# Optimization experiments

Hardware: AMD Instinct MI355X
Metric: run time of the kernel (lower is better)

Reference implementation:

```python
import jax, jax.numpy as jnp
import numpy as np

B, G, C = 32, 512, 768
BG = B * G
H = 12              # MHA heads
MID, H1, N1 = 12, 6, 128   # Attention1 mid dim, heads, fixed block size
AD = 16             # adapter bottleneck
FF = 4 * C
NCLUST = 2048       # 3d grid cells
GRID = 196
D1 = B * GRID       # 1d scatter dim_size
NVIEW = 6
SCALE_FACTOR = 0.5
COEF_PRO = 0.3
EPS = 1e-5


def layernorm(x, g, b):
    m = x.mean(-1, keepdims=True)
    v = x.var(-1, keepdims=True)
    return (x - m) / jnp.sqrt(v + EPS) * g + b


def quick_gelu(x):
    return x * jax.nn.sigmoid(1.702 * x)


def bn_gelu(x, g, b):
    # BatchNorm1d in training mode (batch statistics, biased var) + exact GELU
    m = x.mean(0)
    v = x.var(0)
    y = (x - m) / jnp.sqrt(v + EPS) * g + b
    return jax.nn.gelu(y, approximate=False)


def seg_max_mean(feat, idx, nseg):
    # segment_csr(sorted feat, ptr) == segment reduce over cluster ids; empty segments -> 0
    cnt = jax.ops.segment_sum(jnp.ones((feat.shape[0], 1), feat.dtype), idx, nseg)
    smax = jnp.where(cnt > 0, jax.ops.segment_max(feat, idx, nseg), 0.0)
    smean = jax.ops.segment_sum(feat, idx, nseg) / jnp.maximum(cnt, 1.0)
    return smax, smean


def setup_inputs() -> dict:
    key = jax.random.key(0)
    ks = iter(jax.random.split(key, 40))
    r = lambda shape, s=0.02: jax.random.normal(next(ks), shape, jnp.float32) * s
    return {
        "x": jax.random.normal(next(ks), (B, G + 1, C), jnp.float32),
        "ln1_g": jnp.ones((C,)), "ln1_b": jnp.zeros((C,)),
        "ln2_g": jnp.ones((C,)), "ln2_b": jnp.zeros((C,)),
        "Wqkv": r((3 * C, C)), "bqkv": jnp.zeros((3 * C,)),
        "Wo": r((C, C)), "bo": jnp.zeros((C,)),
        "Wfc": r((FF, C)), "bfc": jnp.zeros((FF,)),
        "Wproj": r((C, FF)), "bproj": jnp.zeros((C,)),
        "Wa1": r((AD, C)), "ba1": jnp.zeros((AD,)),
        "Wa2": r((C, AD)), "ba2": jnp.zeros((C,)),
        "bn3d_g": jnp.ones((C,)), "bn3d_b": jnp.zeros((C,)),
        "bn1d_g": jnp.ones((NVIEW, C)), "bn1d_b": jnp.zeros((NVIEW, C)),
        "n3_g": jnp.ones((NVIEW, C)), "n3_b": jnp.zeros((NVIEW, C)),
        "a1_qkv_w": r((NVIEW, 3 * MID, C)), "a1_qkv_b": jnp.zeros((NVIEW, 3 * MID)),
        "a1_proj_w": r((NVIEW, C, MID)), "a1_proj_b": jnp.zeros((NVIEW, C)),
        "cluster": jax.random.randint(next(ks), (BG,), 0, NCLUST),
        "flat_grid_index": jax.random.randint(next(ks), (NVIEW, BG), 0, D1),
        "mask": jax.random.randint(next(ks), (NVIEW, BG // N1, N1, N1), 0, 2).astype(bool),
    }


def reference(x, ln1_g, ln1_b, ln2_g, ln2_b, Wqkv, bqkv, Wo, bo, Wfc, bfc,
              Wproj, bproj, Wa1, ba1, Wa2, ba2, bn3d_g, bn3d_b, bn1d_g, bn1d_b,
              n3_g, n3_b, a1_qkv_w, a1_qkv_b, a1_proj_w, a1_proj_b,
              cluster, flat_grid_index, mask):
    hd = C // H
    # --- multi-head self-attention over tokens + residual ---
    y = layernorm(x, ln1_g, ln1_b)
    qkv = y @ Wqkv.T + bqkv                          # [B, S, 3C]
    q, k, v = jnp.split(qkv, 3, axis=-1)
    heads = lambda t: t.reshape(B, G + 1, H, hd).transpose(0, 2, 1, 3)
    q, k, v = heads(q), heads(k), heads(v)
    attn = jax.nn.softmax(jnp.einsum('bhqd,bhkd->bhqk', q, k) / jnp.sqrt(jnp.float32(hd)), axis=-1)
    o = jnp.einsum('bhqk,bhkd->bhqd', attn, v).transpose(0, 2, 1, 3).reshape(B, G + 1, C)
    x = x + o @ Wo.T + bo
    # --- MLP (QuickGELU) + scaled adapter ---
    y = layernorm(x, ln2_g, ln2_b)
    x_ffn = quick_gelu(y @ Wfc.T + bfc) @ Wproj.T + bproj
    adapt = quick_gelu(x_ffn @ Wa1.T + ba1) @ Wa2.T + ba2
    x = x + x_ffn + SCALE_FACTOR * adapt
    cls_x = x[:, :1]
    xt = x[:, 1:]                                    # [B, G, C]
    feat = xt.reshape(BG, C)
    # --- 3d cluster pooling: segment max+mean -> BN+GELU -> gather back ---
    fmax, fmean = seg_max_mean(feat, cluster, NCLUST)
    x_3d = bn_gelu(fmax + fmean, bn3d_g, bn3d_b)[cluster].reshape(B, G, C)
    # --- per-view local masked attention + 1d grid scatter pooling (vmapped) ---
    def view_branch(n3g, n3b, qkvw, qkvb, projw, projb, bng, bnb, idx, msk):
        z = layernorm(feat, n3g, n3b)
        qkv1 = (z @ qkvw.T + qkvb).reshape(BG // N1, N1, 3, H1, MID // H1).transpose(2, 0, 3, 1, 4)
        q1, k1, v1 = qkv1[0], qkv1[1], qkv1[2]       # [Bn, H1, N1, hd1]
        a = jnp.einsum('bhqd,bhkd->bhqk', q1, k1) * (MID ** -0.5)
        a = a + jnp.where(msk, -100000.0, 0.0)[:, None]  # mask broadcast over heads
        a = jax.nn.softmax(a, axis=-1)
        o1 = jnp.einsum('bhqk,bhkd->bhqd', a, v1).transpose(0, 2, 1, 3).reshape(BG, MID)
        flat = o1 @ projw.T + projb + feat
        smax, smean = seg_max_mean(flat, idx, D1)
        return bn_gelu(smax + smean, bng, bnb)[idx].reshape(B, G, C)
    pos = jax.vmap(view_branch)(n3_g, n3_b, a1_qkv_w, a1_qkv_b, a1_proj_w, a1_proj_b,
                                bn1d_g, bn1d_b, flat_grid_index, mask)   # [6, B, G, C]
    # --- cosine-similarity-weighted fusion of the 6 views against x_3d ---
    def cossim(a, b):
        na = jnp.maximum(jnp.linalg.norm(a, axis=-1), 1e-8)
        nb = jnp.maximum(jnp.linalg.norm(b, axis=-1), 1e-8)
        return (a * b).sum(-1) / (na * nb)
    sims = (jax.vmap(lambda p: cossim(p, x_3d))(pos) + 1.0) / 2.0        # [6, B, G]
    sims = sims / sims.sum(0, keepdims=True)
    x_sup = (pos * sims[..., None]).sum(0)                               # [B, G, C]
    xt = xt + COEF_PRO * x_sup
    return jnp.concatenate([cls_x, xt], axis=1)
```

## Files before the change

kernel.cpp:

```cpp
#include <hip/hip_runtime.h>
#include <hip/hip_bf16.h>
#include <math.h>

typedef unsigned int u32;
typedef __hip_bfloat16 bf16;
typedef __attribute__((ext_vector_type(8))) short bh8;
typedef __attribute__((ext_vector_type(4))) float fx4;
typedef __attribute__((ext_vector_type(2))) unsigned int u32x2;
typedef __attribute__((ext_vector_type(4))) unsigned int u32x4;

#define CDIM   768
#define BATCH  32
#define SEQ    513
#define NT     (BATCH*SEQ)
#define NR     16384
#define NHEAD  12
#define HD     64
#define FFDIM  3072
#define NCLUST 2048
#define D1SEG  6272
#define NVIEW  6
#define MIDD   12
#define H1N    6
#define N1V    128
#define NB1    128
#define CHROWS 8208

#define A_FS      ((size_t)0)
#define B_FS      ((size_t)6303744)
#define X1_FS     ((size_t)25214976)
#define AH_FS     ((size_t)31518720)
#define D_FS      ((size_t)31781376)
#define DTOT_FS   9640064
#define X3D_FS    ((size_t)(D_FS + DTOT_FS))
#define BNV_FS    (X3D_FS + 1572864)
#define STATM_FS  (BNV_FS + 14450688)
#define STATR_FS  (STATM_FS + 768)
#define DI_CNT    (D_FS)
#define DI_BASE   (D_FS + 6272)
#define DI_CUR    (D_FS + 12544)
#define DI_ORD    (D_FS + 18816)
#define DW_FS     (D_FS + 40960)
#define DWV_FS    (D_FS + 3600000)

__device__ inline float b2f(bf16 v){ return __bfloat162float(v); }
__device__ inline float ldv(const float* p, size_t i){ return p[i]; }
__device__ inline float ldv(const bf16*  p, size_t i){ return __bfloat162float(p[i]); }
__device__ inline void  stv(float* p, size_t i, float v){ p[i] = v; }
__device__ inline void  stv(bf16*  p, size_t i, float v){ p[i] = __float2bfloat16(v); }
__device__ inline short f2bs(float f){ bf16 h = __float2bfloat16(f); return *(short*)&h; }
__device__ inline void gload_lds16(const bf16* g, short* l){
    __builtin_amdgcn_global_load_lds((const __attribute__((address_space(1))) void*)g,
                                     (__attribute__((address_space(3))) void*)l, 16, 0, 0);
}
__device__ inline u32x2 ds_tr16(unsigned a){
    u32x2 d;
    asm volatile("ds_read_b64_tr_b16 %0, %1" : "=v"(d) : "v"(a));
    return d;
}


__global__ __launch_bounds__(256) void k_zero(float* p, int n){
    for (int i = blockIdx.x*256 + threadIdx.x; i < n; i += gridDim.x*256) p[i] = 0.0f;
}

__global__ __launch_bounds__(256) void k_f2b(const float* __restrict__ in, bf16* __restrict__ out, int n){
    for (int i = blockIdx.x*256 + threadIdx.x; i < n; i += gridDim.x*256)
        out[i] = __float2bfloat16(in[i]);
}

template<typename TI>
__global__ __launch_bounds__(256) void k_ln(const TI* __restrict__ in, bf16* __restrict__ out,
                                            const float* __restrict__ g, const float* __restrict__ b){
    int i = blockIdx.x;
    int tid = threadIdx.x;
    const TI* r = in + (size_t)i*CDIM;
    float v0 = ldv(r,(size_t)tid), v1 = ldv(r,(size_t)tid+256), v2 = ldv(r,(size_t)tid+512);
    float s  = v0+v1+v2;
    float s2 = v0*v0+v1*v1+v2*v2;
    __shared__ float t1[4], t2[4];
    #pragma unroll
    for (int o=32;o;o>>=1){ s += __shfl_down(s,o,64); s2 += __shfl_down(s2,o,64); }
    int lane = tid & 63, wid = tid >> 6;
    if (!lane){ t1[wid]=s; t2[wid]=s2; }
    __syncthreads();
    float S  = t1[0]+t1[1]+t1[2]+t1[3];
    float S2 = t2[0]+t2[1]+t2[2]+t2[3];
    float m  = S * (1.0f/CDIM);
    float var = S2 * (1.0f/CDIM) - m*m;
    float rstd = rsqrtf(var + 1e-5f);
    bf16* o_ = out + (size_t)i*CDIM;
    stv(o_,(size_t)tid,     (v0-m)*rstd*g[tid]     + b[tid]);
    stv(o_,(size_t)tid+256, (v1-m)*rstd*g[tid+256] + b[tid+256]);
    stv(o_,(size_t)tid+512, (v2-m)*rstd*g[tid+512] + b[tid+512]);
}

__global__ __launch_bounds__(256) void k_lnn(const float* __restrict__ in, bf16* __restrict__ out){
    int i = blockIdx.x;
    size_t ri = (size_t)(i + (i>>9) + 1);
    int tid = threadIdx.x;
    const float* r = in + ri*CDIM;
    float v0 = r[tid], v1 = r[tid+256], v2 = r[tid+512];
    float s  = v0+v1+v2;
    float s2 = v0*v0+v1*v1+v2*v2;
    __shared__ float t1[4], t2[4];
    #pragma unroll
    for (int o=32;o;o>>=1){ s += __shfl_down(s,o,64); s2 += __shfl_down(s2,o,64); }
    int lane = tid & 63, wid = tid >> 6;
    if (!lane){ t1[wid]=s; t2[wid]=s2; }
    __syncthreads();
    float S  = t1[0]+t1[1]+t1[2]+t1[3];
    float S2 = t2[0]+t2[1]+t2[2]+t2[3];
    float m  = S * (1.0f/CDIM);
    float var = S2 * (1.0f/CDIM) - m*m;
    float rstd = rsqrtf(var + 1e-5f);
    bf16* o_ = out + (size_t)i*CDIM;
    stv(o_,(size_t)tid,     (v0-m)*rstd);
    stv(o_,(size_t)tid+256, (v1-m)*rstd);
    stv(o_,(size_t)tid+512, (v2-m)*rstd);
}

__global__ __launch_bounds__(256) void k_foldw(const float* __restrict__ aqw, const float* __restrict__ aqb,
                                               const float* __restrict__ n3g, const float* __restrict__ n3b,
                                               bf16* __restrict__ Wv, float* __restrict__ bv){
    int row = blockIdx.x;
    int v = row/36;
    const float* w = aqw + (size_t)row*768;
    const float* g = n3g + v*768;
    const float* b = n3b + v*768;
    int tid = threadIdx.x;
    float s = 0.0f;
    #pragma unroll
    for (int j=tid; j<768; j+=256){
        float wv = w[j];
        Wv[(size_t)row*768 + j] = __float2bfloat16(wv*g[j]);
        s += wv*b[j];
    }
    __shared__ float t1[4];
    #pragma unroll
    for (int o=32;o;o>>=1) s += __shfl_down(s,o,64);
    int lane = tid & 63, wid = tid >> 6;
    if (!lane) t1[wid]=s;
    __syncthreads();
    if (tid==0) bv[row] = aqb[row] + t1[0]+t1[1]+t1[2]+t1[3];
}

template<typename TO, int ACT, int RES>
__global__ __launch_bounds__(256) void k_gemm_mfma(const bf16* __restrict__ A, const bf16* __restrict__ W,
                                                   const float* __restrict__ bias, const float* __restrict__ res,
                                                   TO* __restrict__ out, int M, int N, int K){
    __shared__ short As[3][128*32];
    __shared__ short Ws[3][128*32];
    int nbx = (N + 127) >> 7;
    int nwg = gridDim.x;
    int orig = blockIdx.x;
    int xcd = orig & 7, sl = orig >> 3;
    int q8 = nwg >> 3, r8 = nwg & 7;
    int wg = (xcd < r8 ? xcd*(q8+1) : r8*(q8+1) + (xcd - r8)*q8) + sl;
    int by = wg / nbx;
    int bm = by*128, bn = (wg - by*nbx)*128;
    int tid = threadIdx.x, wid = tid>>6, lane = tid&63, quad = lane>>4, l16 = lane&15;
    int wr = (wid>>1)*64, wc = (wid&1)*64;
    fx4 acc[4][4];
    #pragma unroll
    for (int i=0;i<4;i++)
        #pragma unroll
        for (int j=0;j<4;j++) acc[i][j] = (fx4){0.f,0.f,0.f,0.f};
    int lrow = lane>>2;
    int gchunk = (lane&3) ^ ((lane>>3)&3);
    int r0a0 = wid*32 + lrow,  r0a1 = wid*32 + 16 + lrow;
    int ra0 = bm + r0a0; if (ra0 > M-1) ra0 = M-1;
    int ra1 = bm + r0a1; if (ra1 > M-1) ra1 = M-1;
    int rw0 = bn + r0a0; if (rw0 > N-1) rw0 = N-1;
    int rw1 = bn + r0a1; if (rw1 > N-1) rw1 = N-1;
    const bf16* pa0 = A + (size_t)ra0*K + gchunk*8;
    const bf16* pa1 = A + (size_t)ra1*K + gchunk*8;
    const bf16* pw0 = W + (size_t)rw0*K + gchunk*8;
    const bf16* pw1 = W + (size_t)rw1*K + gchunk*8;
    int sL0 = (wid*32)*32;
    int sL1 = (wid*32 + 16)*32;
    int slotx = (l16>>1)&3;
    int nt = K >> 5;
    #define STAGE4(bsel, t) do { int _k0 = (t) << 5;               \
        gload_lds16(pa0 + _k0, &As[(bsel)][sL0]);                  \
        gload_lds16(pa1 + _k0, &As[(bsel)][sL1]);                  \
        gload_lds16(pw0 + _k0, &Ws[(bsel)][sL0]);                  \
        gload_lds16(pw1 + _k0, &Ws[(bsel)][sL1]); } while(0)
    STAGE4(0, 0);
    STAGE4(1, 1);
    int cur = 0;
    for (int t = 0; t < nt; ++t){
        if (t + 1 < nt) asm volatile("s_waitcnt vmcnt(4)" ::: "memory");
        else            asm volatile("s_waitcnt vmcnt(0)" ::: "memory");
        __builtin_amdgcn_s_barrier();
        __builtin_amdgcn_sched_barrier(0);
        const short* Ab = &As[cur][0];
        const short* Wb = &Ws[cur][0];
        bh8 af[4], bf_[4];
        int sa = (quad ^ slotx)*8;
        #pragma unroll
        for (int i=0;i<4;i++) af[i]  = *(const bh8*)&Ab[(wr + i*16 + l16)*32 + sa];
        #pragma unroll
        for (int j=0;j<4;j++) bf_[j] = *(const bh8*)&Wb[(wc + j*16 + l16)*32 + sa];
        if (t + 2 < nt){
            int nb = cur + 2; if (nb >= 3) nb -= 3;
            STAGE4(nb, t + 2);
        }
        #pragma unroll
        for (int i=0;i<4;i++)
            #pragma unroll
            for (int j=0;j<4;j++)
                acc[i][j] = __builtin_amdgcn_mfma_f32_16x16x32_bf16(af[i], bf_[j], acc[i][j], 0,0,0);
        cur += 1; if (cur == 3) cur = 0;
    }
    #undef STAGE4
    #pragma unroll
    for (int i=0;i<4;i++){
        #pragma unroll
        for (int r=0;r<4;r++){
            int row = bm + wr + i*16 + quad*4 + r;
            if (row >= M) continue;
            #pragma unroll
            for (int j=0;j<4;j++){
                int col = bn + wc + j*16 + l16;
                if (col >= N) continue;
                float v = acc[i][j][r] + bias[col];
                if (ACT == 1) v = v / (1.0f + __expf(-1.702f*v));
                if (RES) v += res[(size_t)row*N + col];
                stv(out, (size_t)row*N + col, v);
            }
        }
    }
}

#define KSTR 72
__global__ __launch_bounds__(256) void k_attn_mfma(const bf16* __restrict__ qkv, bf16* __restrict__ obuf){
    __shared__ short Ks[2][64*KSTR];
    __shared__ short Vs[2][64*KSTR];
    __shared__ short Ps[4*16*KSTR];
    int id = blockIdx.x;
    int qt = (id>>3) % 9;
    int bh = (id&7) + ((id/72)<<3);
    int h = bh % NHEAD, b = bh / NHEAD;
    int tid = threadIdx.x, wid = tid>>6, lane = tid&63, quad = lane>>4, l16 = lane&15;
    size_t base = (size_t)b*SEQ*2304;
    int q_own = qt*64 + wid*16 + l16;
    int q_cl  = q_own > 512 ? 512 : q_own;
    const bf16* qrow = qkv + base + (size_t)q_cl*2304 + h*HD;
    bh8 qa0 = *(const bh8*)(qrow + quad*8);
    bh8 qa1 = *(const bh8*)(qrow + 32 + quad*8);
    {
        union { bh8 v; short s[8]; } u0, u1;
        u0.v = qa0; u1.v = qa1;
        #pragma unroll
        for (int j=0;j<8;j++){
            bf16 a = *(bf16*)&u0.s[j]; u0.s[j] = f2bs(0.125f*b2f(a));
            bf16 c = *(bf16*)&u1.s[j]; u1.s[j] = f2bs(0.125f*b2f(c));
        }
        qa0 = u0.v; qa1 = u1.v;
    }
    fx4 o[4];
    #pragma unroll
    for (int d=0; d<4; d++) o[d] = (fx4){0.f,0.f,0.f,0.f};
    float mrow[4] = {-1e30f,-1e30f,-1e30f,-1e30f};
    float lrow[4] = {0.f,0.f,0.f,0.f};
    int srow = tid>>2, d0 = (tid&3)*16;
    int s_st = (srow>>2)*4 + (tid&3);
    int vsb  = (s_st ^ ((srow>>3)<<1))*KSTR + (srow&3)*16;
    int h8 = l16>>3, l7 = l16&7;
    short* psw[4];
    #pragma unroll
    for (int nt=0;nt<4;nt++)
        psw[nt] = &Ps[(wid*16 + quad*4)*KSTR + (((nt<<1)|h8) ^ (quad<<1))*8 + l7];
    int swr = (l16>>2)<<1;
    const short* prd0 = &Ps[(wid*16+l16)*KSTR + ((quad ^ swr))*8];
    const short* prd1 = &Ps[(wid*16+l16)*KSTR + (((4|quad) ^ swr))*8];
    unsigned vls = (unsigned)(size_t)(__attribute__((address_space(3))) short*)&Vs[0][0] + 2u*l16;
    #define TRA(vb,hf,c,dt) ((vb) + 144u*(unsigned)(((32*(hf) + 8*quad + 4*(c) + (dt)) ^ (8*(hf) + 2*quad))))
    bh8 kv0, kv1, vv0, vv1;
    {
        const bf16* krow = qkv + base + 768 + (size_t)srow*2304 + h*HD + d0;
        kv0 = *(const bh8*)(krow);
        kv1 = *(const bh8*)(krow + 8);
        vv0 = *(const bh8*)(krow + 768);
        vv1 = *(const bh8*)(krow + 776);
    }
    int p = 0;
    for (int kt=0; kt<9; kt++){
        short* KsP = &Ks[p][0];
        short* VsP = &Vs[p][0];
        *(bh8*)&KsP[srow*KSTR + d0]     = kv0;
        *(bh8*)&KsP[srow*KSTR + d0 + 8] = kv1;
        *(bh8*)&VsP[vsb]     = vv0;
        *(bh8*)&VsP[vsb + 8] = vv1;
        __syncthreads();
        if (kt < 8){
            int kg = (kt+1)*64 + srow; if (kg > 512) kg = 512;
            const bf16* krow = qkv + base + 768 + (size_t)kg*2304 + h*HD + d0;
            kv0 = *(const bh8*)(krow);
            kv1 = *(const bh8*)(krow + 8);
            vv0 = *(const bh8*)(krow + 768);
            vv1 = *(const bh8*)(krow + 776);
        }
        unsigned vb = vls + 9216u*(unsigned)p;
        fx4 s[4];
        __builtin_amdgcn_s_setprio(1);
        #pragma unroll
        for (int nt=0; nt<4; nt++){
            bh8 kb0 = *(const bh8*)&KsP[(nt*16+l16)*KSTR + quad*8];
            bh8 kb1 = *(const bh8*)&KsP[(nt*16+l16)*KSTR + 32 + quad*8];
            fx4 a = (fx4){0.f,0.f,0.f,0.f};
            a = __builtin_amdgcn_mfma_f32_16x16x32_bf16(qa0, kb0, a, 0,0,0);
            a = __builtin_amdgcn_mfma_f32_16x16x32_bf16(qa1, kb1, a, 0,0,0);
            s[nt] = a;
        }
        __builtin_amdgcn_s_setprio(0);
        u32x2 tv[16];
        #pragma unroll
        for (int dt=0; dt<4; dt++){
            tv[dt*4+0] = ds_tr16(TRA(vb,0,0,dt));
            tv[dt*4+1] = ds_tr16(TRA(vb,0,1,dt));
            tv[dt*4+2] = ds_tr16(TRA(vb,1,0,dt));
            tv[dt*4+3] = ds_tr16(TRA(vb,1,1,dt));
        }
        float tmax[4] = {-1e30f,-1e30f,-1e30f,-1e30f};
        if (kt < 8){
            #pragma unroll
            for (int nt=0; nt<4; nt++)
                #pragma unroll
                for (int r=0;r<4;r++) tmax[r] = fmaxf(tmax[r], s[nt][r]);
        } else {
            #pragma unroll
            for (int nt=0; nt<4; nt++){
                bool ok = (nt==0) && (l16==0);
                #pragma unroll
                for (int r=0;r<4;r++){
                    float v = ok ? s[nt][r] : -1e30f;
                    s[nt][r] = v;
                    tmax[r] = fmaxf(tmax[r], v);
                }
            }
        }
        #pragma unroll
        for (int msk=1; msk<16; msk<<=1)
            #pragma unroll
            for (int r=0;r<4;r++) tmax[r] = fmaxf(tmax[r], __shfl_xor(tmax[r], msk, 64));
        bool grow = (tmax[0]>mrow[0])|(tmax[1]>mrow[1])|(tmax[2]>mrow[2])|(tmax[3]>mrow[3]);
        if (__any(grow)){
            #pragma unroll
            for (int r=0;r<4;r++){
                float mn = fmaxf(mrow[r], tmax[r]);
                float al = __expf(mrow[r] - mn);
                mrow[r] = mn;
                lrow[r] *= al;
                #pragma unroll
                for (int d=0; d<4; d++) o[d][r] *= al;
            }
        }
        float ps[4] = {0.f,0.f,0.f,0.f};
        #pragma unroll
        for (int nt=0; nt<4; nt++)
            #pragma unroll
            for (int r=0;r<4;r++){
                float pp = __expf(s[nt][r] - mrow[r]);
                s[nt][r] = pp;
                ps[r] += pp;
            }
        #pragma unroll
        for (int msk=1; msk<16; msk<<=1)
            #pragma unroll
            for (int r=0;r<4;r++) ps[r] += __shfl_xor(ps[r], msk, 64);
        #pragma unroll
        for (int r=0;r<4;r++) lrow[r] += ps[r];
        #pragma unroll
        for (int nt=0; nt<4; nt++)
            #pragma unroll
            for (int r=0;r<4;r++) psw[nt][r*KSTR] = f2bs(s[nt][r]);
        bh8 pa0 = *(const bh8*)prd0;
        bh8 pa1 = *(const bh8*)prd1;
        asm volatile("s_waitcnt lgkmcnt(0)" ::: "memory");
        __builtin_amdgcn_sched_barrier(0);
        __builtin_amdgcn_s_setprio(1);
        #pragma unroll
        for (int dt=0; dt<4; dt++){
            union { u32x4 u; bh8 h; } v0, v1;
            v0.u = (u32x4){tv[dt*4+0][0], tv[dt*4+0][1], tv[dt*4+1][0], tv[dt*4+1][1]};
            v1.u = (u32x4){tv[dt*4+2][0], tv[dt*4+2][1], tv[dt*4+3][0], tv[dt*4+3][1]};
            o[dt] = __builtin_amdgcn_mfma_f32_16x16x32_bf16(pa0, v0.h, o[dt], 0,0,0);
            o[dt] = __builtin_amdgcn_mfma_f32_16x16x32_bf16(pa1, v1.h, o[dt], 0,0,0);
        }
        __builtin_amdgcn_s_setprio(0);
        p ^= 1;
    }
    #undef TRA
    float inv[4];
    #pragma unroll
    for (int r=0;r<4;r++) inv[r] = 1.0f/lrow[r];
    #pragma unroll
    for (int r=0;r<4;r++){
        int q = qt*64 + wid*16 + quad*4 + r;
        if (q < SEQ){
            size_t ob = ((size_t)(b*SEQ+q))*CDIM + h*HD;
            #pragma unroll
            for (int dt=0; dt<4; dt++)
                obuf[ob + dt*16 + l16] = __float2bfloat16(o[dt][r]*inv[r]);
        }
    }
}

__global__ __launch_bounds__(256) void k_comb(const bf16* __restrict__ x1, const bf16* __restrict__ xffn,
                                              const float* __restrict__ ah, const float* __restrict__ Wa2,
                                              const float* __restrict__ ba2, float* __restrict__ x2){
    int i = blockIdx.x; int tid = threadIdx.x;
    __shared__ float ar[16];
    if (tid < 16) ar[tid] = ah[(size_t)i*16 + tid];
    __syncthreads();
    for (int c=tid; c<CDIM; c+=256){
        const float* w = Wa2 + (size_t)c*16;
        float a = ba2[c];
        #pragma unroll
        for (int mm=0; mm<16; mm++) a += ar[mm]*w[mm];
        size_t o = (size_t)i*CDIM + c;
        x2[o] = b2f(x1[o]) + b2f(xffn[o]) + 0.5f*a;
    }
}

__global__ __launch_bounds__(256) void k_icount(const int* __restrict__ idx, int* __restrict__ cnt, int n){
    int i = blockIdx.x*256 + threadIdx.x;
    if (i < n) atomicAdd(&cnt[idx[i]], 1);
}

__global__ __launch_bounds__(256) void k_iscan(const int* __restrict__ cnt, int* __restrict__ base,
                                               int* __restrict__ cur, int nseg){
    __shared__ int part[256], off[256];
    int t = threadIdx.x;
    int chunk = (nseg + 255) >> 8;
    int j0 = t*chunk, j1 = j0 + chunk; if (j1 > nseg) j1 = nseg;
    int s = 0;
    for (int j=j0; j<j1; j++) s += cnt[j];
    part[t] = s; __syncthreads();
    if (t == 0){ int acc=0; for (int i=0;i<256;i++){ off[i]=acc; acc+=part[i]; } }
    __syncthreads();
    int acc = off[t];
    for (int j=j0; j<j1; j++){ base[j]=acc; cur[j]=acc; acc+=cnt[j]; }
}

__global__ __launch_bounds__(256) void k_iscatter(const int* __restrict__ idx, int* __restrict__ cur,
                                                  int* __restrict__ order, int n){
    int i = blockIdx.x*256 + threadIdx.x;
    if (i < n){
        int pos = atomicAdd(&cur[idx[i]], 1);
        order[pos] = i;
    }
}

__global__ __launch_bounds__(256) void k_icount6(const int* __restrict__ fgi, int* __restrict__ cnt){
    int g = blockIdx.x*256 + threadIdx.x;
    int v = g >> 14;
    atomicAdd(&cnt[v*D1SEG + fgi[g]], 1);
}

__global__ __launch_bounds__(256) void k_iscan6(const int* __restrict__ cnt, int* __restrict__ base,
                                                int* __restrict__ cur){
    __shared__ int part[256], off[256];
    int v = blockIdx.x;
    const int* c = cnt + v*D1SEG;
    int* bs = base + v*D1SEG;
    int* cu = cur + v*D1SEG;
    int t = threadIdx.x;
    int chunk = (D1SEG + 255) >> 8;
    int j0 = t*chunk, j1 = j0 + chunk; if (j1 > D1SEG) j1 = D1SEG;
    int s = 0;
    for (int j=j0; j<j1; j++) s += c[j];
    part[t] = s; __syncthreads();
    if (t == 0){ int acc=0; for (int i=0;i<256;i++){ off[i]=acc; acc+=part[i]; } }
    __syncthreads();
    int acc = off[t];
    for (int j=j0; j<j1; j++){ bs[j]=acc; cu[j]=acc; acc+=c[j]; }
}

__global__ __launch_bounds__(256) void k_iscatter6(const int* __restrict__ fgi, int* __restrict__ cur,
                                                   int* __restrict__ order){
    int g = blockIdx.x*256 + threadIdx.x;
    int v = g >> 14;
    int pos = atomicAdd(&cur[v*D1SEG + fgi[g]], 1);
    order[(size_t)v*NR + pos] = g & (NR-1);
}

__global__ __launch_bounds__(256) void k_gather_seg(const float* __restrict__ outx, const int* __restrict__ basep,
                                                    const int* __restrict__ cntp, const int* __restrict__ order,
                                                    float* __restrict__ dst){
    int sg = blockIdx.x; int tid = threadIdx.x;
    int n = cntp[sg], b0 = basep[sg];
    float mx[3] = {-1e30f,-1e30f,-1e30f};
    float sm[3] = {0.f,0.f,0.f};
    for (int r=0; r<n; r++){
        int i = order[b0+r];
        size_t rb = (size_t)(i + (i>>9) + 1)*CDIM;
        #pragma unroll
        for (int j=0;j<3;j++){
            float v = outx[rb + tid + j*256];
            mx[j] = fmaxf(mx[j], v); sm[j] += v;
        }
    }
    float den = (float)(n > 1 ? n : 1);
    size_t db = (size_t)sg*CDIM;
    #pragma unroll
    for (int j=0;j<3;j++)
        dst[db + tid + j*256] = (n > 0 ? mx[j] : 0.f) + sm[j]/den;
}

__global__ __launch_bounds__(256) void k_gather_flat(const float* __restrict__ outx, const float* __restrict__ o1v,
                                                     const float* __restrict__ Wp, const float* __restrict__ bp,
                                                     const int* __restrict__ basep, const int* __restrict__ cntp,
                                                     const int* __restrict__ order, float* __restrict__ dst){
    int sg = blockIdx.x; int tid = threadIdx.x;
    int n = cntp[sg], b0 = basep[sg];
    float w[3][MIDD], bb[3];
    #pragma unroll
    for (int j=0;j<3;j++){
        int c = tid + j*256;
        bb[j] = bp[c];
        #pragma unroll
        for (int mm=0;mm<MIDD;mm++) w[j][mm] = Wp[(size_t)c*MIDD + mm];
    }
    float mx[3] = {-1e30f,-1e30f,-1e30f};
    float sm[3] = {0.f,0.f,0.f};
    for (int r=0; r<n; r++){
        int i = order[b0+r];
        const float* orow = o1v + (size_t)i*MIDD;
        float ov[MIDD];
        #pragma unroll
        for (int mm=0;mm<MIDD;mm++) ov[mm] = orow[mm];
        size_t rb = (size_t)(i + (i>>9) + 1)*CDIM;
        #pragma unroll
        for (int j=0;j<3;j++){
            float a = bb[j];
            #pragma unroll
            for (int mm=0;mm<MIDD;mm++) a += ov[mm]*w[j][mm];
            a += outx[rb + tid + j*256];
            mx[j] = fmaxf(mx[j], a); sm[j] += a;
        }
    }
    float den = (float)(n > 1 ? n : 1);
    size_t db = (size_t)sg*CDIM;
    #pragma unroll
    for (int j=0;j<3;j++)
        dst[db + tid + j*256] = (n > 0 ? mx[j] : 0.f) + sm[j]/den;
}

__global__ __launch_bounds__(256) void k_colstats_part(const float* __restrict__ in, int rows,
                                                       float* __restrict__ sumv, float* __restrict__ sumsq){
    int c = blockIdx.x*256 + threadIdx.x;
    if (c >= CDIM) return;
    int chunk = (rows + 31) >> 5;
    int r0 = blockIdx.y*chunk;
    int r1 = r0 + chunk; if (r1 > rows) r1 = rows;
    float s = 0.0f, s2 = 0.0f;
    for (int r=r0; r<r1; r++){
        float v = in[(size_t)r*CDIM + c];
        s += v; s2 += v*v;
    }
    atomicAdd(&sumv[c], s);
    atomicAdd(&sumsq[c], s2);
}

template<typename TO>
__global__ __launch_bounds__(256) void k_bngelu2(const float* __restrict__ in, TO* __restrict__ outp,
                                                 const float* __restrict__ sv, const float* __restrict__ sq,
                                                 const float* __restrict__ g, const float* __restrict__ b,
                                                 int n, float invn){
    int i = blockIdx.x*256 + threadIdx.x;
    if (i >= n) return;
    int c = i - (i/CDIM)*CDIM;
    float m = sv[c]*invn;
    float var = sq[c]*invn - m*m;
    float r = rsqrtf(fmaxf(var, 0.0f) + 1e-5f);
    float y = (in[i]-m)*r*g[c] + b[c];
    stv(outp, (size_t)i, 0.5f*y*(1.0f + erff(y*0.70710678118654752f)));
}

#define MSTR 33
__global__ __launch_bounds__(256) void k_attnv(const float* __restrict__ qkv1a,
                                               const unsigned char* __restrict__ mask,
                                               float* __restrict__ o1all){
    __shared__ float Qs[N1V][13], Ksv[N1V][13], Vsv[N1V][13];
    __shared__ int   Ms[N1V*MSTR];
    int blk = blockIdx.x, v = blockIdx.y;
    int tid = threadIdx.x;
    if (tid < N1V){
        const float4* rp = (const float4*)(qkv1a + (size_t)(blk*N1V + tid)*216 + v*36);
        #pragma unroll
        for (int j=0;j<3;j++){
            float4 q4 = rp[j], k4 = rp[3+j], v4 = rp[6+j];
            Qs[tid][j*4+0]=q4.x; Qs[tid][j*4+1]=q4.y; Qs[tid][j*4+2]=q4.z; Qs[tid][j*4+3]=q4.w;
            Ksv[tid][j*4+0]=k4.x; Ksv[tid][j*4+1]=k4.y; Ksv[tid][j*4+2]=k4.z; Ksv[tid][j*4+3]=k4.w;
            Vsv[tid][j*4+0]=v4.x; Vsv[tid][j*4+1]=v4.y; Vsv[tid][j*4+2]=v4.z; Vsv[tid][j*4+3]=v4.w;
        }
    }
    {
        const int4* mp = (const int4*)(mask + ((size_t)v*NB1 + blk)*N1V*N1V);
        #pragma unroll
        for (int it=0; it<4; it++){
            int e = tid + it*256;
            int4 m4 = mp[e];
            int row = e >> 3, c4 = (e & 7)*4;
            Ms[row*MSTR + c4 + 0] = m4.x;
            Ms[row*MSTR + c4 + 1] = m4.y;
            Ms[row*MSTR + c4 + 2] = m4.z;
            Ms[row*MSTR + c4 + 3] = m4.w;
        }
    }
    __syncthreads();
    int n = tid & 127, hg = tid >> 7;
    const float scale = 0.28867513459481287f;
    #pragma unroll
    for (int hh=0; hh<3; hh++){
        int h = hg*3 + hh;
        float q0 = Qs[n][h*2], q1 = Qs[n][h*2+1];
        float m = -1e30f;
        #pragma unroll 4
        for (int k4=0; k4<32; k4++){
            int mw = Ms[n*MSTR + k4];
            #pragma unroll
            for (int j=0;j<4;j++){
                int k = k4*4 + j;
                float s = (q0*Ksv[k][h*2] + q1*Ksv[k][h*2+1])*scale + (((mw>>(j*8))&0xFF) ? -100000.0f : 0.0f);
                m = fmaxf(m, s);
            }
        }
        float l = 0.f, o0 = 0.f, o1v = 0.f;
        #pragma unroll 4
        for (int k4=0; k4<32; k4++){
            int mw = Ms[n*MSTR + k4];
            #pragma unroll
            for (int j=0;j<4;j++){
                int k = k4*4 + j;
                float s = (q0*Ksv[k][h*2] + q1*Ksv[k][h*2+1])*scale + (((mw>>(j*8))&0xFF) ? -100000.0f : 0.0f);
                float p = __expf(s - m);
                l += p; o0 += p*Vsv[k][h*2]; o1v += p*Vsv[k][h*2+1];
            }
        }
        float inv = 1.0f/l;
        float* orow = o1all + ((size_t)v*NR + blk*N1V + n)*MIDD + h*2;
        orow[0] = o0*inv; orow[1] = o1v*inv;
    }
}

__global__ __launch_bounds__(256) void k_final(float* __restrict__ outx, const float* __restrict__ x3d,
                                               const bf16* __restrict__ bnv, const int* __restrict__ cluster,
                                               const int* __restrict__ fgi){
    int i = blockIdx.x; int tid = threadIdx.x;
    int cl = cluster[i];
    const float* xr = x3d + (size_t)cl*CDIM;
    const bf16* pr[NVIEW];
    #pragma unroll
    for (int v=0; v<NVIEW; v++)
        pr[v] = bnv + ((size_t)v*D1SEG + fgi[(size_t)v*NR + i])*CDIM;
    size_t rb = (size_t)(i + (i>>9) + 1)*CDIM;
    float pv[NVIEW][3], ft[3];
    float dotv[NVIEW] = {0,0,0,0,0,0};
    float np2[NVIEW]  = {0,0,0,0,0,0};
    float nx2 = 0.0f;
    #pragma unroll
    for (int j=0; j<3; j++){
        int c = tid + j*256;
        float xv = xr[c]; nx2 += xv*xv;
        ft[j] = outx[rb + c];
        #pragma unroll
        for (int v=0; v<NVIEW; v++){
            float p = b2f(pr[v][c]); pv[v][j] = p;
            dotv[v] += p*xv; np2[v] += p*p;
        }
    }
    __shared__ float part[4*13];
    __shared__ float ssim[NVIEW];
    float vals[13];
    vals[0] = nx2;
    #pragma unroll
    for (int v=0; v<NVIEW; v++){ vals[1+v] = dotv[v]; vals[7+v] = np2[v]; }
    int lane = tid & 63, wid = tid >> 6;
    #pragma unroll
    for (int k=0; k<13; k++){
        float w = vals[k];
        #pragma unroll
        for (int o=32;o;o>>=1) w += __shfl_down(w,o,64);
        if (!lane) part[wid*13 + k] = w;
    }
    __syncthreads();
    if (tid == 0){
        float tot[13];
        #pragma unroll
        for (int k=0; k<13; k++) tot[k] = part[k] + part[13+k] + part[26+k] + part[39+k];
        float nb = fmaxf(sqrtf(tot[0]), 1e-8f);
        float sv[NVIEW]; float ssumv = 0.0f;
        #pragma unroll
        for (int v=0; v<NVIEW; v++){
            float na = fmaxf(sqrtf(tot[7+v]), 1e-8f);
            float cs = tot[1+v] / (na*nb);
            sv[v] = (cs + 1.0f)*0.5f;
            ssumv += sv[v];
        }
        #pragma unroll
        for (int v=0; v<NVIEW; v++) ssim[v] = sv[v]/ssumv;
    }
    __syncthreads();
    #pragma unroll
    for (int j=0; j<3; j++){
        int c = tid + j*256;
        float xs = 0.0f;
        #pragma unroll
        for (int v=0; v<NVIEW; v++) xs += ssim[v]*pv[v][j];
        outx[rb + c] = ft[j] + 0.3f*xs;
    }
}

extern "C" void kernel_launch(void* const* d_in, const int* in_sizes, int n_in,
                              void* d_out, int out_size, void* d_ws, size_t ws_size,
                              hipStream_t stream){
    const float* x     = (const float*)d_in[0];
    const float* ln1g  = (const float*)d_in[1];
    const float* ln1b  = (const float*)d_in[2];
    const float* ln2g  = (const float*)d_in[3];
    const float* ln2b  = (const float*)d_in[4];
    const float* Wqkv  = (const float*)d_in[5];
    const float* bqkv  = (const float*)d_in[6];
    const float* Wo    = (const float*)d_in[7];
    const float* bo    = (const float*)d_in[8];
    const float* Wfc   = (const float*)d_in[9];
    const float* bfc   = (const float*)d_in[10];
    const float* Wproj = (const float*)d_in[11];
    const float* bproj = (const float*)d_in[12];
    const float* Wa1   = (const float*)d_in[13];
    const float* ba1   = (const float*)d_in[14];
    const float* Wa2   = (const float*)d_in[15];
    const float* ba2   = (const float*)d_in[16];
    const float* bn3dg = (const float*)d_in[17];
    const float* bn3db = (const float*)d_in[18];
    const float* bn1dg = (const float*)d_in[19];
    const float* bn1db = (const float*)d_in[20];
    const float* n3g   = (const float*)d_in[21];
    const float* n3b   = (const float*)d_in[22];
    const float* aqw   = (const float*)d_in[23];
    const float* aqb   = (const float*)d_in[24];
    const float* apw   = (const float*)d_in[25];
    const float* apb   = (const float*)d_in[26];
    const int*   cluster = (const int*)d_in[27];
    const int*   fgi     = (const int*)d_in[28];
    const unsigned char* mask = (const unsigned char*)d_in[29];
    float* out = (float*)d_out;
    float* ws  = (float*)d_ws;

    bf16*  yb    = (bf16*)(ws + A_FS);
    bf16*  qkvb  = (bf16*)(ws + B_FS);
    bf16*  hb    = (bf16*)(ws + B_FS);
    bf16*  xffb  = (bf16*)(ws + B_FS + 12607488);
    float* qkv1a = ws + B_FS;
    float* o1all = ws + B_FS + 3538944;
    float* svs   = ws + B_FS + 4718592;
    bf16*  x1b   = (bf16*)(ws + X1_FS);
    float* ah    = ws + AH_FS;
    int*   icnt  = (int*)(ws + DI_CNT);
    int*   ibase = (int*)(ws + DI_BASE);
    int*   icur  = (int*)(ws + DI_CUR);
    int*   iord  = (int*)(ws + DI_ORD);
    float* x3d   = ws + X3D_FS;
    bf16*  bnv   = (bf16*)(ws + BNV_FS);
    float* statm = ws + STATM_FS;
    float* statr = ws + STATR_FS;
    bf16* WqkvB  = (bf16*)(ws + DW_FS);
    bf16* WoB    = WqkvB + 2304*768;
    bf16* WfcB   = WoB   + 768*768;
    bf16* WprojB = WfcB  + 3072*768;
    bf16* WvB    = (bf16*)(ws + DWV_FS);
    float* bvP   = ws + DWV_FS + 82944;
    bf16* Wa1B   = (bf16*)(ws + DWV_FS + 83200);
    int*   icnt6  = (int*)(ws + AH_FS);
    int*   ibase6 = icnt6 + 6*D1SEG;
    int*   icur6  = ibase6 + 6*D1SEG;
    int*   iord6  = icur6 + 6*D1SEG;
    float* stat6  = (float*)(iord6 + 6*NR);

    k_f2b<<<1024, 256, 0, stream>>>(Wqkv,  WqkvB,  2304*768);
    k_f2b<<<1024, 256, 0, stream>>>(Wo,    WoB,    768*768);
    k_f2b<<<1024, 256, 0, stream>>>(Wfc,   WfcB,   3072*768);
    k_f2b<<<1024, 256, 0, stream>>>(Wproj, WprojB, 768*3072);
    k_f2b<<<48, 256, 0, stream>>>(Wa1, Wa1B, 16*768);
    k_foldw<<<216, 256, 0, stream>>>(aqw, aqb, n3g, n3b, WvB, bvP);
    k_ln<float><<<NT, 256, 0, stream>>>(x, yb, ln1g, ln1b);
    k_gemm_mfma<bf16,0,0><<<(2304/128)*((NT+127)/128), 256, 0, stream>>>(yb, WqkvB, bqkv, nullptr, qkvb, NT, 2304, 768);
    k_attn_mfma<<<3456, 256, 0, stream>>>(qkvb, yb);
    k_gemm_mfma<bf16,0,1><<<(768/128)*((NT+127)/128), 256, 0, stream>>>(yb, WoB, bo, x, x1b, NT, 768, 768);
    k_ln<bf16><<<NT, 256, 0, stream>>>(x1b, yb, ln2g, ln2b);
    for (int cch=0; cch<2; cch++){
        const bf16* a2 = yb + (size_t)cch*CHROWS*CDIM;
        bf16* xo = xffb + (size_t)cch*CHROWS*CDIM;
        k_gemm_mfma<bf16,1,0><<<(FFDIM/128)*((CHROWS+127)/128), 256, 0, stream>>>(a2, WfcB, bfc, nullptr, hb, CHROWS, FFDIM, 768);
        k_gemm_mfma<bf16,0,0><<<(768/128)*((CHROWS+127)/128), 256, 0, stream>>>(hb, WprojB, bproj, nullptr, xo, CHROWS, 768, FFDIM);
    }
    k_gemm_mfma<float,1,0><<<1*((NT+127)/128), 256, 0, stream>>>(xffb, Wa1B, ba1, nullptr, ah, NT, 16, 768);
    k_comb<<<NT, 256, 0, stream>>>(x1b, xffb, ah, Wa2, ba2, out);
    k_zero<<<32, 256, 0, stream>>>((float*)icnt, NCLUST);
    k_icount<<<NR/256, 256, 0, stream>>>(cluster, icnt, NR);
    k_iscan<<<1, 256, 0, stream>>>(icnt, ibase, icur, NCLUST);
    k_iscatter<<<NR/256, 256, 0, stream>>>(cluster, icur, iord, NR);
    k_gather_seg<<<NCLUST, 256, 0, stream>>>(out, ibase, icnt, iord, x3d);
    k_zero<<<6, 256, 0, stream>>>(statm, 1536);
    k_colstats_part<<<dim3(3, 32), 256, 0, stream>>>(x3d, NCLUST, statm, statr);
    k_bngelu2<float><<<(NCLUST*CDIM+255)/256, 256, 0, stream>>>(x3d, x3d, statm, statr, bn3dg, bn3db,
                                                                NCLUST*CDIM, 1.0f/NCLUST);
    k_lnn<<<NR, 256, 0, stream>>>(out, yb);
    k_gemm_mfma<float,0,0><<<2*(NR/128), 256, 0, stream>>>(yb, WvB, bvP, nullptr, qkv1a, NR, 216, 768);
    k_attnv<<<dim3(NB1, NVIEW), 256, 0, stream>>>(qkv1a, mask, o1all);
    k_zero<<<(6*D1SEG+255)/256, 256, 0, stream>>>((float*)icnt6, 6*D1SEG);
    k_icount6<<<6*NR/256, 256, 0, stream>>>(fgi, icnt6);
    k_iscan6<<<6, 256, 0, stream>>>(icnt6, ibase6, icur6);
    k_iscatter6<<<6*NR/256, 256, 0, stream>>>(fgi, icur6, iord6);
    k_zero<<<(9216+255)/256, 256, 0, stream>>>(stat6, 9216);
    for (int v=0; v<NVIEW; v++){
        k_gather_flat<<<D1SEG, 256, 0, stream>>>(out, o1all + (size_t)v*NR*MIDD,
                                                 apw + (size_t)v*CDIM*MIDD, apb + (size_t)v*CDIM,
                                                 ibase6 + v*D1SEG, icnt6 + v*D1SEG, iord6 + (size_t)v*NR, svs);
        k_colstats_part<<<dim3(3, 32), 256, 0, stream>>>(svs, D1SEG, stat6 + v*1536, stat6 + v*1536 + 768);
        k_bngelu2<bf16><<<(D1SEG*CDIM+255)/256, 256, 0, stream>>>(svs, bnv + (size_t)v*D1SEG*CDIM,
                                                                  stat6 + v*1536, stat6 + v*1536 + 768,
                                                                  bn1dg + v*CDIM, bn1db + v*CDIM,
                                                                  D1SEG*CDIM, 1.0f/D1SEG);
    }
    k_final<<<NR, 256, 0, stream>>>(out, x3d, bnv, cluster, fgi);
}
```

Measured before the change: 1.597 ms.

## Transpose attention scores to simplify softmax, merge conversion and zero launches

```diff
diff --git a/kernel.cpp b/kernel.cpp
--- a/kernel.cpp
+++ b/kernel.cpp
@@ -58,15 +58,28 @@
     asm volatile("ds_read_b64_tr_b16 %0, %1" : "=v"(d) : "v"(a));
     return d;
 }
+__device__ inline unsigned cvtpk_bf16(float lo, float hi){
+    unsigned r;
+    asm("v_cvt_pk_bf16_f32 %0, %1, %2" : "=v"(r) : "v"(lo), "v"(hi));
+    return r;
+}
 
 
 __global__ __launch_bounds__(256) void k_zero(float* p, int n){
     for (int i = blockIdx.x*256 + threadIdx.x; i < n; i += gridDim.x*256) p[i] = 0.0f;
 }
 
-__global__ __launch_bounds__(256) void k_f2b(const float* __restrict__ in, bf16* __restrict__ out, int n){
-    for (int i = blockIdx.x*256 + threadIdx.x; i < n; i += gridDim.x*256)
-        out[i] = __float2bfloat16(in[i]);
+__global__ __launch_bounds__(256) void k_f2b5(const float* __restrict__ a0, bf16* __restrict__ b0, int n0,
+                                              const float* __restrict__ a1, bf16* __restrict__ b1, int n1,
+                                              const float* __restrict__ a2, bf16* __restrict__ b2, int n2,
+                                              const float* __restrict__ a3, bf16* __restrict__ b3, int n3,
+                                              const float* __restrict__ a4, bf16* __restrict__ b4, int n4){
+    int i0 = blockIdx.x*256 + threadIdx.x, st = gridDim.x*256;
+    for (int i=i0; i<n0; i+=st) b0[i] = __float2bfloat16(a0[i]);
+    for (int i=i0; i<n1; i+=st) b1[i] = __float2bfloat16(a1[i]);
+    for (int i=i0; i<n2; i+=st) b2[i] = __float2bfloat16(a2[i]);
+    for (int i=i0; i<n3; i+=st) b3[i] = __float2bfloat16(a3[i]);
+    for (int i=i0; i<n4; i+=st) b4[i] = __float2bfloat16(a4[i]);
 }
 
 template<typename TI>
@@ -194,6 +207,10 @@
         else            asm volatile("s_waitcnt vmcnt(0)" ::: "memory");
         __builtin_amdgcn_s_barrier();
         __builtin_amdgcn_sched_barrier(0);
+        if (t + 2 < nt){
+            int nb = cur + 2; if (nb >= 3) nb -= 3;
+            STAGE4(nb, t + 2);
+        }
         const short* Ab = &As[cur][0];
         const short* Wb = &Ws[cur][0];
         bh8 af[4], bf_[4];
@@ -202,10 +219,6 @@
         for (int i=0;i<4;i++) af[i]  = *(const bh8*)&Ab[(wr + i*16 + l16)*32 + sa];
         #pragma unroll
         for (int j=0;j<4;j++) bf_[j] = *(const bh8*)&Wb[(wc + j*16 + l16)*32 + sa];
-        if (t + 2 < nt){
-            int nb = cur + 2; if (nb >= 3) nb -= 3;
-            STAGE4(nb, t + 2);
-        }
         #pragma unroll
         for (int i=0;i<4;i++)
             #pragma unroll
@@ -262,19 +275,13 @@
     fx4 o[4];
     #pragma unroll
     for (int d=0; d<4; d++) o[d] = (fx4){0.f,0.f,0.f,0.f};
-    float mrow[4] = {-1e30f,-1e30f,-1e30f,-1e30f};
-    float lrow[4] = {0.f,0.f,0.f,0.f};
+    float mrow = -1e30f, lrow = 0.f;
     int srow = tid>>2, d0 = (tid&3)*16;
     int s_st = (srow>>2)*4 + (tid&3);
     int vsb  = (s_st ^ ((srow>>3)<<1))*KSTR + (srow&3)*16;
-    int h8 = l16>>3, l7 = l16&7;
-    short* psw[4];
-    #pragma unroll
-    for (int nt=0;nt<4;nt++)
-        psw[nt] = &Ps[(wid*16 + quad*4)*KSTR + (((nt<<1)|h8) ^ (quad<<1))*8 + l7];
-    int swr = (l16>>2)<<1;
-    const short* prd0 = &Ps[(wid*16+l16)*KSTR + ((quad ^ swr))*8];
-    const short* prd1 = &Ps[(wid*16+l16)*KSTR + (((4|quad) ^ swr))*8];
+    short* pw = &Ps[(wid*16 + l16)*KSTR];
+    const short* prd0 = &Ps[(wid*16+l16)*KSTR + quad*8];
+    const short* prd1 = &Ps[(wid*16+l16)*KSTR + 32 + quad*8];
     unsigned vls = (unsigned)(size_t)(__attribute__((address_space(3))) short*)&Vs[0][0] + 2u*l16;
     #define TRA(vb,hf,c,dt) ((vb) + 144u*(unsigned)(((32*(hf) + 8*quad + 4*(c) + (dt)) ^ (8*(hf) + 2*quad))))
     bh8 kv0, kv1, vv0, vv1;
@@ -310,8 +317,8 @@
             bh8 kb0 = *(const bh8*)&KsP[(nt*16+l16)*KSTR + quad*8];
             bh8 kb1 = *(const bh8*)&KsP[(nt*16+l16)*KSTR + 32 + quad*8];
             fx4 a = (fx4){0.f,0.f,0.f,0.f};
-            a = __builtin_amdgcn_mfma_f32_16x16x32_bf16(qa0, kb0, a, 0,0,0);
-            a = __builtin_amdgcn_mfma_f32_16x16x32_bf16(qa1, kb1, a, 0,0,0);
+            a = __builtin_amdgcn_mfma_f32_16x16x32_bf16(kb0, qa0, a, 0,0,0);
+            a = __builtin_amdgcn_mfma_f32_16x16x32_bf16(kb1, qa1, a, 0,0,0);
             s[nt] = a;
         }
         __builtin_amdgcn_s_setprio(0);
@@ -323,59 +330,54 @@
             tv[dt*4+2] = ds_tr16(TRA(vb,1,0,dt));
             tv[dt*4+3] = ds_tr16(TRA(vb,1,1,dt));
         }
-        float tmax[4] = {-1e30f,-1e30f,-1e30f,-1e30f};
-        if (kt < 8){
+        if (kt == 8){
             #pragma unroll
             for (int nt=0; nt<4; nt++)
                 #pragma unroll
-                for (int r=0;r<4;r++) tmax[r] = fmaxf(tmax[r], s[nt][r]);
-        } else {
-            #pragma unroll
-            for (int nt=0; nt<4; nt++){
-                bool ok = (nt==0) && (l16==0);
+                for (int r=0;r<4;r++){
+                    bool ok = (nt==0) && (r==0) && (quad==0);
+                    s[nt][r] = ok ? s[nt][r] : -1e30f;
+                }
+        }
+        float ml = s[0][0];
+        #pragma unroll
+        for (int nt=0; nt<4; nt++)
+            #pragma unroll
+            for (int r=0;r<4;r++) if (nt|r) ml = fmaxf(ml, s[nt][r]);
+        ml = fmaxf(ml, __shfl_xor(ml, 16, 64));
+        ml = fmaxf(ml, __shfl_xor(ml, 32, 64));
+        if (__any(ml > mrow)){
+            float mn = fmaxf(mrow, ml);
+            float al = __expf(mrow - mn);
+            mrow = mn;
+            lrow *= al;
+            float alr[4];
+            #pragma unroll
+            for (int r=0;r<4;r++) alr[r] = __shfl(al, quad*4 + r, 16);
+            #pragma unroll
+            for (int d=0; d<4; d++)
                 #pragma unroll
-                for (int r=0;r<4;r++){
-                    float v = ok ? s[nt][r] : -1e30f;
-                    s[nt][r] = v;
-                    tmax[r] = fmaxf(tmax[r], v);
-                }
+                for (int r=0;r<4;r++) o[d][r] *= alr[r];
+        }
+        float ps = 0.f;
+        #pragma unroll
+        for (int nt=0; nt<4; nt++)
+            #pragma unroll
+            for (int r=0;r<4;r++){
+                float pp = __expf(s[nt][r] - mrow);
+                s[nt][r] = pp;
+                ps += pp;
             }
-        }
-        #pragma unroll
-        for (int msk=1; msk<16; msk<<=1)
-            #pragma unroll
-            for (int r=0;r<4;r++) tmax[r] = fmaxf(tmax[r], __shfl_xor(tmax[r], msk, 64));
-        bool grow = (tmax[0]>mrow[0])|(tmax[1]>mrow[1])|(tmax[2]>mrow[2])|(tmax[3]>mrow[3]);
-        if (__any(grow)){
-            #pragma unroll
-            for (int r=0;r<4;r++){
-                float mn = fmaxf(mrow[r], tmax[r]);
-                float al = __expf(mrow[r] - mn);
-                mrow[r] = mn;
-                lrow[r] *= al;
-                #pragma unroll
-                for (int d=0; d<4; d++) o[d][r] *= al;
-            }
-        }
-        float ps[4] = {0.f,0.f,0.f,0.f};
-        #pragma unroll
-        for (int nt=0; nt<4; nt++)
-            #pragma unroll
-            for (int r=0;r<4;r++){
-                float pp = __expf(s[nt][r] - mrow[r]);
-                s[nt][r] = pp;
-                ps[r] += pp;
-            }
-        #pragma unroll
-        for (int msk=1; msk<16; msk<<=1)
-            #pragma unroll
-            for (int r=0;r<4;r++) ps[r] += __shfl_xor(ps[r], msk, 64);
-        #pragma unroll
-        for (int r=0;r<4;r++) lrow[r] += ps[r];
-        #pragma unroll
-        for (int nt=0; nt<4; nt++)
-            #pragma unroll
-            for (int r=0;r<4;r++) psw[nt][r*KSTR] = f2bs(s[nt][r]);
+        ps += __shfl_xor(ps, 16, 64);
+        ps += __shfl_xor(ps, 32, 64);
+        lrow += ps;
+        #pragma unroll
+        for (int nt=0; nt<4; nt++){
+            u32x2 w;
+            w[0] = cvtpk_bf16(s[nt][0], s[nt][1]);
+            w[1] = cvtpk_bf16(s[nt][2], s[nt][3]);
+            *(u32x2*)&pw[nt*16 + quad*4] = w;
+        }
         bh8 pa0 = *(const bh8*)prd0;
         bh8 pa1 = *(const bh8*)prd1;
         asm volatile("s_waitcnt lgkmcnt(0)" ::: "memory");
@@ -393,9 +395,9 @@
         p ^= 1;
     }
     #undef TRA
-    float inv[4];
-    #pragma unroll
-    for (int r=0;r<4;r++) inv[r] = 1.0f/lrow[r];
+    float linv[4];
+    #pragma unroll
+    for (int r=0;r<4;r++) linv[r] = 1.0f / __shfl(lrow, quad*4 + r, 16);
     #pragma unroll
     for (int r=0;r<4;r++){
         int q = qt*64 + wid*16 + quad*4 + r;
@@ -403,7 +405,7 @@
             size_t ob = ((size_t)(b*SEQ+q))*CDIM + h*HD;
             #pragma unroll
             for (int dt=0; dt<4; dt++)
-                obuf[ob + dt*16 + l16] = __float2bfloat16(o[dt][r]*inv[r]);
+                obuf[ob + dt*16 + l16] = __float2bfloat16(o[dt][r]*linv[r]);
         }
     }
 }
@@ -781,11 +783,9 @@
     int*   iord6  = icur6 + 6*D1SEG;
     float* stat6  = (float*)(iord6 + 6*NR);
 
-    k_f2b<<<1024, 256, 0, stream>>>(Wqkv,  WqkvB,  2304*768);
-    k_f2b<<<1024, 256, 0, stream>>>(Wo,    WoB,    768*768);
-    k_f2b<<<1024, 256, 0, stream>>>(Wfc,   WfcB,   3072*768);
-    k_f2b<<<1024, 256, 0, stream>>>(Wproj, WprojB, 768*3072);
-    k_f2b<<<48, 256, 0, stream>>>(Wa1, Wa1B, 16*768);
+    k_f2b5<<<2048, 256, 0, stream>>>(Wqkv, WqkvB, 2304*768,  Wo, WoB, 768*768,
+                                     Wfc, WfcB, 3072*768,    Wproj, WprojB, 768*3072,
+                                     Wa1, Wa1B, 16*768);
     k_foldw<<<216, 256, 0, stream>>>(aqw, aqb, n3g, n3b, WvB, bvP);
     k_ln<float><<<NT, 256, 0, stream>>>(x, yb, ln1g, ln1b);
     k_gemm_mfma<bf16,0,0><<<(2304/128)*((NT+127)/128), 256, 0, stream>>>(yb, WqkvB, bqkv, nullptr, qkvb, NT, 2304, 768);
@@ -812,11 +812,10 @@
     k_lnn<<<NR, 256, 0, stream>>>(out, yb);
     k_gemm_mfma<float,0,0><<<2*(NR/128), 256, 0, stream>>>(yb, WvB, bvP, nullptr, qkv1a, NR, 216, 768);
     k_attnv<<<dim3(NB1, NVIEW), 256, 0, stream>>>(qkv1a, mask, o1all);
-    k_zero<<<(6*D1SEG+255)/256, 256, 0, stream>>>((float*)icnt6, 6*D1SEG);
+    k_zero<<<(220416+255)/256, 256, 0, stream>>>((float*)icnt6, 220416);
     k_icount6<<<6*NR/256, 256, 0, stream>>>(fgi, icnt6);
     k_iscan6<<<6, 256, 0, stream>>>(icnt6, ibase6, icur6);
     k_iscatter6<<<6*NR/256, 256, 0, stream>>>(fgi, icur6, iord6);
-    k_zero<<<(9216+255)/256, 256, 0, stream>>>(stat6, 9216);
     for (int v=0; v<NVIEW; v++){
         k_gather_flat<<<D1SEG, 256, 0, stream>>>(out, o1all + (size_t)v*NR*MIDD,
                                                  apw + (size_t)v*CDIM*MIDD, apb + (size_t)v*CDIM,
```

After: 1.592 ms. No clear change (-0.3%).
